# Optimization experiments

Hardware: AMD Instinct MI355X
Metric: run time of the kernel (lower is better)

Reference implementation:

```python
import jax, jax.numpy as jnp
import numpy as np

B, R, SR, K, F = 1, 2048, 24, 8, 32
DIST_FREQ = 2   # dist_xyz_freq -> PE dim 2*2*3 = 12
VIEW_FREQ = 4   # num_viewdir_freqs -> PE dim 2*4*3 = 24


def pe(x, n_freqs):
    # positional encoding: concat sin/cos of x * 2^i, flattened over last dim
    fb = (2.0 ** jnp.arange(n_freqs)).astype(x.dtype)          # [L]
    xb = x[..., None] * fb                                      # [..., 3, L]
    enc = jnp.concatenate([jnp.sin(xb), jnp.cos(xb)], axis=-1)  # [..., 3, 2L]
    return enc.reshape(*x.shape[:-1], -1)                       # [..., 3*2L]


def setup_inputs() -> dict:
    key = jax.random.key(0)
    ks = jax.random.split(key, 12)
    s = 0.1  # small init scale for weights
    return {
        'sampled_embedding': jax.random.normal(ks[0], (B, R, SR, K, F), jnp.float32),
        'dists': jax.random.normal(ks[1], (B, R, SR, K, 3), jnp.float32) * 0.1,
        'viewdirs': jax.random.normal(ks[2], (B, R, SR, 3), jnp.float32),
        'pnt_mask': jax.random.randint(ks[3], (B, R, SR, K), 0, 2, jnp.int32),
        'w1': jax.random.normal(ks[4], (F + 2 * DIST_FREQ * 3, 256), jnp.float32) * s,
        'b1': jnp.zeros((256,), jnp.float32),
        'w2': jax.random.normal(ks[5], (256, 256), jnp.float32) * s,
        'b2': jnp.zeros((256,), jnp.float32),
        'wa1': jax.random.normal(ks[6], (256, 256), jnp.float32) * s,
        'ba1': jnp.zeros((256,), jnp.float32),
        'wa2': jax.random.normal(ks[7], (256, 1), jnp.float32) * s,
        'ba2': jnp.zeros((1,), jnp.float32),
        'wc1': jax.random.normal(ks[8], (256 + 2 * VIEW_FREQ * 3, 256), jnp.float32) * s,
        'bc1': jnp.zeros((256,), jnp.float32),
        'wc2': jax.random.normal(ks[9], (256, 3), jnp.float32) * s,
        'bc2': jnp.zeros((3,), jnp.float32),
    }


def reference(sampled_embedding, dists, viewdirs, pnt_mask,
              w1, b1, w2, b2, wa1, ba1, wa2, ba2, wc1, bc1, wc2, bc2):
    mask = pnt_mask.astype(sampled_embedding.dtype)             # [B,R,SR,K]

    # quadric distance kernel -> normalized neighbor weights
    d2 = jnp.sum(dists * dists, axis=-1)                        # [B,R,SR,K]
    w = 1.0 / jnp.clip(d2, 1e-8)
    w = w * mask
    w = w / jnp.clip(jnp.sum(w, axis=-1, keepdims=True), 1e-8)  # agg_weight_norm

    # per-neighbor feature MLP (block1): feat ++ PE(dist_xyz) -> 256 -> 256
    feat_in = jnp.concatenate([sampled_embedding, pe(dists, DIST_FREQ)], axis=-1)
    h = jax.nn.relu(feat_in @ w1 + b1)
    h = jax.nn.relu(h @ w2 + b2)                                # [B,R,SR,K,256]

    # distance-weighted aggregation over neighbors (apply_pnt_mask folded into w)
    agg = jnp.einsum('brsk,brskc->brsc', w, h)                  # [B,R,SR,256]

    # alpha branch + raw2out_density (act_super: softplus(raw - 1))
    ah = jax.nn.relu(agg @ wa1 + ba1)
    density = jax.nn.softplus(ah @ wa2 + ba2 - 1.0)             # [B,R,SR,1]

    # color branch + raw2out_color (widened sigmoid)
    cin = jnp.concatenate([agg, pe(viewdirs, VIEW_FREQ)], axis=-1)
    ch = jax.nn.relu(cin @ wc1 + bc1)
    color = jax.nn.sigmoid(ch @ wc2 + bc2) * (1.0 + 2e-3) - 1e-3  # [B,R,SR,3]

    return jnp.concatenate([density, color], axis=-1)           # [B,R,SR,4]
```

## Files before the change

kernel.cpp:

```cpp
#include <hip/hip_runtime.h>

typedef unsigned short ushort_t;
typedef __bf16 bf16x8 __attribute__((ext_vector_type(8)));
typedef float f32x4 __attribute__((ext_vector_type(4)));

#define NPTS   49152
#define KNBR   8
#define PTS_A  8
#define NBLK_A (NPTS / PTS_A)
#define PTS_B  32
#define NBLK_B (NPTS / PTS_B)

#define W1S_OFF   0
#define W2S_OFF   16384
#define WA1S_OFF  81920
#define WC1S_OFF  147456
#define WA2S_OFF  221184
#define WC2S_OFF  225280
#define WS_WEIGHT 229376
#define AGG_OFF   229376

__device__ __forceinline__ float b2f(ushort_t u) {
    return __builtin_bit_cast(float, ((unsigned)u) << 16);
}
__device__ __forceinline__ ushort_t f2b(float f) {
    unsigned x = __builtin_bit_cast(unsigned, f);
    unsigned r = x + 0x7fffu + ((x >> 16) & 1u);
    return (ushort_t)(r >> 16);
}
__device__ __forceinline__ ushort_t f2bc(float f) {
    unsigned x = __builtin_bit_cast(unsigned, f);
    return (ushort_t)((x + 0x8000u) >> 16);
}

__global__ __launch_bounds__(256) void prep_swizzle(
    const float* __restrict__ w1, const float* __restrict__ w2,
    const float* __restrict__ wa1, const float* __restrict__ wc1,
    const float* __restrict__ wa2, const float* __restrict__ wc2,
    ushort_t* __restrict__ ws)
{
    int idx = blockIdx.x * 256 + threadIdx.x;
    if (idx >= WS_WEIGHT) return;

    if (idx >= WA2S_OFF) {
        int off2 = idx - WA2S_OFF;
        int mat = off2 >> 12;
        int off = off2 & 4095;
        int kb = off >> 7, rem = off & 127;
        int n = rem >> 3, j = rem & 7;
        int k = kb * 8 + j;
        float v = 0.f;
        if (mat == 0) { if (n == 0) v = wa2[k]; }
        else          { if (n < 3)  v = wc2[k * 3 + n]; }
        ws[idx] = f2b(v);
        return;
    }

    const float* src; int off, srcK, base;
    if (idx < W2S_OFF)        { src = w1;  base = W1S_OFF;  off = idx - W1S_OFF;  srcK = 44;  }
    else if (idx < WA1S_OFF)  { src = w2;  base = W2S_OFF;  off = idx - W2S_OFF;  srcK = 256; }
    else if (idx < WC1S_OFF)  { src = wa1; base = WA1S_OFF; off = idx - WA1S_OFF; srcK = 256; }
    else                      { src = wc1; base = WC1S_OFF; off = idx - WC1S_OFF; srcK = 280; }
    int kb  = off >> 11;
    int rem = off & 2047;
    int j = rem >> 8;
    int n = rem & 255;
    int k = kb * 8 + j;
    float v = (k < srcK) ? src[k * 256 + n] : 0.f;
    ws[base + kb * 2048 + n * 8 + j] = f2b(v);
}

__global__ __launch_bounds__(256) void pa_mlp(
    const float* __restrict__ emb, const float* __restrict__ dists,
    const int* __restrict__ mask,  const float* __restrict__ b1,
    const float* __restrict__ b2,  const ushort_t* __restrict__ ws,
    ushort_t* __restrict__ aggg)
{
    __shared__ __align__(16) ushort_t uH1[64 * 264];
    __shared__ __align__(16) float sWraw[64];
    __shared__ __align__(16) float sWn[64];
    ushort_t (*sFeat)[72] = (ushort_t(*)[72])uH1;
    ushort_t (*sH1)[264]  = (ushort_t(*)[264])uH1;

    const int tid  = threadIdx.x;
    const int lane = tid & 63;
    const int wv   = tid >> 6;
    const int n0   = lane & 15;
    const int quad = lane >> 4;
    const int pb   = blockIdx.x * PTS_A;
    const int colB = wv * 64;

    {
        int g0 = blockIdx.x * 2048 + tid * 8;
        int r = tid >> 2, c8 = (tid & 3) * 8;
        float4 f0 = *(const float4*)(emb + g0);
        float4 f1 = *(const float4*)(emb + g0 + 4);
        ushort_t v8[8];
        v8[0] = f2bc(f0.x); v8[1] = f2bc(f0.y); v8[2] = f2bc(f0.z); v8[3] = f2bc(f0.w);
        v8[4] = f2bc(f1.x); v8[5] = f2bc(f1.y); v8[6] = f2bc(f1.z); v8[7] = f2bc(f1.w);
        *(uint4*)&sFeat[r][c8] = *(uint4*)v8;
    }
    if (tid < 64) {
        int gr = pb * KNBR + tid;
        float x = dists[gr * 3 + 0];
        float y = dists[gr * 3 + 1];
        float z = dists[gr * 3 + 2];
        float d2 = x * x + y * y + z * z;
        sWraw[tid] = (float)mask[gr] / fmaxf(d2, 1e-8f);
        float xs[3] = {x, y, z};
        #pragma unroll
        for (int d = 0; d < 3; d++) {
            #pragma unroll
            for (int l = 0; l < 2; l++) {
                float ang = xs[d] * (float)(1 << l);
                sFeat[tid][32 + d * 4 + l]     = f2bc(__sinf(ang));
                sFeat[tid][32 + d * 4 + 2 + l] = f2bc(__cosf(ang));
            }
        }
        #pragma unroll
        for (int c = 44; c < 64; c++) sFeat[tid][c] = 0;
    }
    __syncthreads();
    if (tid < 64) {
        int lp = tid >> 3;
        float s = 0.f;
        #pragma unroll
        for (int k = 0; k < 8; k++) s += sWraw[lp * 8 + k];
        sWn[tid] = sWraw[tid] / fmaxf(s, 1e-8f);
    }

    f32x4 acc[16];
    #pragma unroll
    for (int i = 0; i < 16; i++) acc[i] = (f32x4){0.f, 0.f, 0.f, 0.f};

    #pragma unroll
    for (int ki = 0; ki < 2; ki++) {
        bf16x8 a[4];
        #pragma unroll
        for (int mt = 0; mt < 4; mt++)
            a[mt] = *(const bf16x8*)&sFeat[mt * 16 + n0][ki * 32 + quad * 8];
        const ushort_t* bp = ws + W1S_OFF + ki * 8192 + quad * 2048 + (colB + n0) * 8;
        #pragma unroll
        for (int nt = 0; nt < 4; nt++) {
            bf16x8 b = *(const bf16x8*)(bp + nt * 128);
            #pragma unroll
            for (int mt = 0; mt < 4; mt++)
                acc[mt * 4 + nt] = __builtin_amdgcn_mfma_f32_16x16x32_bf16(a[mt], b, acc[mt * 4 + nt], 0, 0, 0);
        }
    }
    __syncthreads();

    {
        #pragma unroll
        for (int nt = 0; nt < 4; nt++) {
            int col = colB + nt * 16 + n0;
            float bias = b1[col];
            #pragma unroll
            for (int mt = 0; mt < 4; mt++)
                #pragma unroll
                for (int r = 0; r < 4; r++)
                    sH1[mt * 16 + quad * 4 + r][col] = f2bc(fmaxf(acc[mt * 4 + nt][r] + bias, 0.f));
        }
    }
    __syncthreads();

    #pragma unroll
    for (int i = 0; i < 16; i++) acc[i] = (f32x4){0.f, 0.f, 0.f, 0.f};
    #pragma unroll
    for (int ki = 0; ki < 8; ki++) {
        bf16x8 a[4];
        #pragma unroll
        for (int mt = 0; mt < 4; mt++)
            a[mt] = *(const bf16x8*)&sH1[mt * 16 + n0][ki * 32 + quad * 8];
        const ushort_t* bp = ws + W2S_OFF + ki * 8192 + quad * 2048 + (colB + n0) * 8;
        #pragma unroll
        for (int nt = 0; nt < 4; nt++) {
            bf16x8 b = *(const bf16x8*)(bp + nt * 128);
            #pragma unroll
            for (int mt = 0; mt < 4; mt++)
                acc[mt * 4 + nt] = __builtin_amdgcn_mfma_f32_16x16x32_bf16(a[mt], b, acc[mt * 4 + nt], 0, 0, 0);
        }
    }
    {
        #pragma unroll
        for (int mt = 0; mt < 4; mt++) {
            f32x4 wn4 = *(const f32x4*)&sWn[mt * 16 + quad * 4];
            #pragma unroll
            for (int nt = 0; nt < 4; nt++) {
                int col = colB + nt * 16 + n0;
                float bias = b2[col];
                float s = fmaxf(acc[mt * 4 + nt][0] + bias, 0.f) * wn4[0]
                        + fmaxf(acc[mt * 4 + nt][1] + bias, 0.f) * wn4[1]
                        + fmaxf(acc[mt * 4 + nt][2] + bias, 0.f) * wn4[2]
                        + fmaxf(acc[mt * 4 + nt][3] + bias, 0.f) * wn4[3];
                s += __shfl_xor(s, 16);
                if ((quad & 1) == 0) {
                    int pt = pb + 2 * mt + (quad >> 1);
                    aggg[(size_t)pt * 256 + col] = f2bc(s);
                }
            }
        }
    }
}

__global__ __launch_bounds__(256) void pa_branch(
    const float* __restrict__ vdirs,
    const float* __restrict__ ba1v, const float* __restrict__ ba2v,
    const float* __restrict__ bc1v, const float* __restrict__ bc2v,
    const ushort_t* __restrict__ ws, const ushort_t* __restrict__ aggg,
    float* __restrict__ out)
{
    __shared__ __align__(16) ushort_t reg1[32 * 296];
    __shared__ __align__(16) ushort_t reg2[32 * 264];
    ushort_t (*sCin)[296] = (ushort_t(*)[296])reg1;
    ushort_t (*sAh)[264]  = (ushort_t(*)[264])reg1;
    ushort_t (*sCh)[264]  = (ushort_t(*)[264])reg2;

    const int tid  = threadIdx.x;
    const int lane = tid & 63;
    const int wv   = tid >> 6;
    const int n0   = lane & 15;
    const int quad = lane >> 4;
    const int pb   = blockIdx.x * PTS_B;
    const int colB = wv * 64;

    #pragma unroll
    for (int it = 0; it < 4; it++) {
        int idx = (tid + it * 256) * 8;
        uint4 v = *(const uint4*)(aggg + (size_t)pb * 256 + idx);
        *(uint4*)&sCin[idx >> 8][idx & 255] = v;
    }
    #pragma unroll
    for (int it = 0; it < 3; it++) {
        int t = tid + it * 256;
        int p = t / 24, j = t % 24;
        int d = j >> 3, jj = j & 7, l = jj & 3, isc = jj >> 2;
        float ang = vdirs[(pb + p) * 3 + d] * (float)(1 << l);
        sCin[p][256 + j] = f2bc(isc ? __cosf(ang) : __sinf(ang));
    }
    sCin[tid >> 3][280 + (tid & 7)] = 0;
    __syncthreads();

    f32x4 accA[8], accC[8];
    #pragma unroll
    for (int i = 0; i < 8; i++) { accA[i] = (f32x4){0.f, 0.f, 0.f, 0.f}; accC[i] = accA[i]; }

    #pragma unroll
    for (int ki = 0; ki < 8; ki++) {
        bf16x8 a0 = *(const bf16x8*)&sCin[n0][ki * 32 + quad * 8];
        bf16x8 a1 = *(const bf16x8*)&sCin[16 + n0][ki * 32 + quad * 8];
        const ushort_t* bp = ws + WA1S_OFF + ki * 8192 + quad * 2048 + (colB + n0) * 8;
        #pragma unroll
        for (int nt = 0; nt < 4; nt++) {
            bf16x8 b = *(const bf16x8*)(bp + nt * 128);
            accA[nt]     = __builtin_amdgcn_mfma_f32_16x16x32_bf16(a0, b, accA[nt], 0, 0, 0);
            accA[4 + nt] = __builtin_amdgcn_mfma_f32_16x16x32_bf16(a1, b, accA[4 + nt], 0, 0, 0);
        }
    }
    #pragma unroll
    for (int ki = 0; ki < 9; ki++) {
        bf16x8 a0 = *(const bf16x8*)&sCin[n0][ki * 32 + quad * 8];
        bf16x8 a1 = *(const bf16x8*)&sCin[16 + n0][ki * 32 + quad * 8];
        const ushort_t* bp = ws + WC1S_OFF + ki * 8192 + quad * 2048 + (colB + n0) * 8;
        #pragma unroll
        for (int nt = 0; nt < 4; nt++) {
            bf16x8 b = *(const bf16x8*)(bp + nt * 128);
            accC[nt]     = __builtin_amdgcn_mfma_f32_16x16x32_bf16(a0, b, accC[nt], 0, 0, 0);
            accC[4 + nt] = __builtin_amdgcn_mfma_f32_16x16x32_bf16(a1, b, accC[4 + nt], 0, 0, 0);
        }
    }
    __syncthreads();

    #pragma unroll
    for (int nt = 0; nt < 4; nt++) {
        int col = colB + nt * 16 + n0;
        float biasA = ba1v[col];
        float biasC = bc1v[col];
        #pragma unroll
        for (int mt = 0; mt < 2; mt++)
            #pragma unroll
            for (int r = 0; r < 4; r++) {
                int row = mt * 16 + quad * 4 + r;
                sAh[row][col] = f2bc(fmaxf(accA[mt * 4 + nt][r] + biasA, 0.f));
                sCh[row][col] = f2bc(fmaxf(accC[mt * 4 + nt][r] + biasC, 0.f));
            }
    }
    __syncthreads();

    {
        const int isColor = wv >> 1;
        const int baseM   = (wv & 1) * 16;
        const ushort_t* A = isColor ? &sCh[0][0] : &sAh[0][0];
        const ushort_t* B = ws + (isColor ? WC2S_OFF : WA2S_OFF);
        f32x4 acc4 = (f32x4){0.f, 0.f, 0.f, 0.f};
        #pragma unroll
        for (int ki = 0; ki < 8; ki++) {
            bf16x8 a = *(const bf16x8*)(A + (baseM + n0) * 264 + ki * 32 + quad * 8);
            bf16x8 b = *(const bf16x8*)(B + ki * 512 + quad * 128 + n0 * 8);
            acc4 = __builtin_amdgcn_mfma_f32_16x16x32_bf16(a, b, acc4, 0, 0, 0);
        }
        if (!isColor) {
            if (n0 == 0) {
                float ba2s = ba2v[0];
                #pragma unroll
                for (int r = 0; r < 4; r++) {
                    int gp = pb + baseM + quad * 4 + r;
                    float yv = acc4[r] + ba2s - 1.0f;
                    out[(size_t)gp * 4] = (yv > 20.f) ? yv : log1pf(expf(yv));
                }
            }
        } else {
            if (n0 < 3) {
                float bc2s = bc2v[n0];
                #pragma unroll
                for (int r = 0; r < 4; r++) {
                    int gp = pb + baseM + quad * 4 + r;
                    float sig = 1.f / (1.f + expf(-(acc4[r] + bc2s)));
                    out[(size_t)gp * 4 + 1 + n0] = sig * (1.0f + 2e-3f) - 1e-3f;
                }
            }
        }
    }
}

extern "C" void kernel_launch(void* const* d_in, const int* in_sizes, int n_in,
                              void* d_out, int out_size, void* d_ws, size_t ws_size,
                              hipStream_t stream) {
    const float* emb   = (const float*)d_in[0];
    const float* dists = (const float*)d_in[1];
    const float* vdir  = (const float*)d_in[2];
    const int*   mask  = (const int*)d_in[3];
    const float* w1    = (const float*)d_in[4];
    const float* b1    = (const float*)d_in[5];
    const float* w2    = (const float*)d_in[6];
    const float* b2    = (const float*)d_in[7];
    const float* wa1   = (const float*)d_in[8];
    const float* ba1   = (const float*)d_in[9];
    const float* wa2   = (const float*)d_in[10];
    const float* ba2   = (const float*)d_in[11];
    const float* wc1   = (const float*)d_in[12];
    const float* bc1   = (const float*)d_in[13];
    const float* wc2   = (const float*)d_in[14];
    const float* bc2   = (const float*)d_in[15];
    ushort_t* ws  = (ushort_t*)d_ws;
    float*    out = (float*)d_out;

    prep_swizzle<<<dim3((WS_WEIGHT + 255) / 256), dim3(256), 0, stream>>>(
        w1, w2, wa1, wc1, wa2, wc2, ws);
    pa_mlp<<<dim3(NBLK_A), dim3(256), 0, stream>>>(
        emb, dists, mask, b1, b2, ws, ws + AGG_OFF);
    pa_branch<<<dim3(NBLK_B), dim3(256), 0, stream>>>(
        vdir, ba1, ba2, bc1, bc2, ws, ws + AGG_OFF, out);
}
```

Before: 211.0 us.

## Make pa_mlp persistent with register-cached W2 and bias folded into W1

```diff
diff --git a/kernel.cpp b/kernel.cpp
--- a/kernel.cpp
+++ b/kernel.cpp
@@ -4,12 +4,13 @@
 typedef __bf16 bf16x8 __attribute__((ext_vector_type(8)));
 typedef float f32x4 __attribute__((ext_vector_type(4)));
 
-#define NPTS   49152
-#define KNBR   8
-#define PTS_A  8
-#define NBLK_A (NPTS / PTS_A)
-#define PTS_B  32
-#define NBLK_B (NPTS / PTS_B)
+#define NPTS    49152
+#define KNBR    8
+#define PTS_A   8
+#define PBLK_A  512
+#define ITERS_A 12
+#define PTS_B   32
+#define NBLK_B  (NPTS / PTS_B)
 
 #define W1S_OFF   0
 #define W2S_OFF   16384
@@ -34,7 +35,8 @@
 }
 
 __global__ __launch_bounds__(256) void prep_swizzle(
-    const float* __restrict__ w1, const float* __restrict__ w2,
+    const float* __restrict__ w1, const float* __restrict__ b1,
+    const float* __restrict__ w2,
     const float* __restrict__ wa1, const float* __restrict__ wc1,
     const float* __restrict__ wa2, const float* __restrict__ wc2,
     ushort_t* __restrict__ ws)
@@ -56,9 +58,20 @@
         return;
     }
 
-    const float* src; int off, srcK, base;
-    if (idx < W2S_OFF)        { src = w1;  base = W1S_OFF;  off = idx - W1S_OFF;  srcK = 44;  }
-    else if (idx < WA1S_OFF)  { src = w2;  base = W2S_OFF;  off = idx - W2S_OFF;  srcK = 256; }
+    int off, base;
+    if (idx < W2S_OFF) {
+        off = idx; base = W1S_OFF;
+        int kb = off >> 11, rem = off & 2047;
+        int j = rem >> 8, n = rem & 255;
+        int k = kb * 8 + j;
+        float v = 0.f;
+        if (k < 44)       v = w1[k * 256 + n];
+        else if (k == 44) v = b1[n];
+        ws[base + kb * 2048 + n * 8 + j] = f2b(v);
+        return;
+    }
+    const float* src; int srcK;
+    if (idx < WA1S_OFF)       { src = w2;  base = W2S_OFF;  off = idx - W2S_OFF;  srcK = 256; }
     else if (idx < WC1S_OFF)  { src = wa1; base = WA1S_OFF; off = idx - WA1S_OFF; srcK = 256; }
     else                      { src = wc1; base = WC1S_OFF; off = idx - WC1S_OFF; srcK = 280; }
     int kb  = off >> 11;
@@ -70,11 +83,10 @@
     ws[base + kb * 2048 + n * 8 + j] = f2b(v);
 }
 
-__global__ __launch_bounds__(256) void pa_mlp(
+__global__ __launch_bounds__(256, 2) void pa_mlp(
     const float* __restrict__ emb, const float* __restrict__ dists,
-    const int* __restrict__ mask,  const float* __restrict__ b1,
-    const float* __restrict__ b2,  const ushort_t* __restrict__ ws,
-    ushort_t* __restrict__ aggg)
+    const int* __restrict__ mask,  const float* __restrict__ b2,
+    const ushort_t* __restrict__ ws, ushort_t* __restrict__ aggg)
 {
     __shared__ __align__(16) ushort_t uH1[64 * 264];
     __shared__ __align__(16) float sWraw[64];
@@ -87,119 +99,129 @@
     const int wv   = tid >> 6;
     const int n0   = lane & 15;
     const int quad = lane >> 4;
-    const int pb   = blockIdx.x * PTS_A;
     const int colB = wv * 64;
 
-    {
-        int g0 = blockIdx.x * 2048 + tid * 8;
-        int r = tid >> 2, c8 = (tid & 3) * 8;
-        float4 f0 = *(const float4*)(emb + g0);
-        float4 f1 = *(const float4*)(emb + g0 + 4);
-        ushort_t v8[8];
-        v8[0] = f2bc(f0.x); v8[1] = f2bc(f0.y); v8[2] = f2bc(f0.z); v8[3] = f2bc(f0.w);
-        v8[4] = f2bc(f1.x); v8[5] = f2bc(f1.y); v8[6] = f2bc(f1.z); v8[7] = f2bc(f1.w);
-        *(uint4*)&sFeat[r][c8] = *(uint4*)v8;
-    }
-    if (tid < 64) {
-        int gr = pb * KNBR + tid;
-        float x = dists[gr * 3 + 0];
-        float y = dists[gr * 3 + 1];
-        float z = dists[gr * 3 + 2];
-        float d2 = x * x + y * y + z * z;
-        sWraw[tid] = (float)mask[gr] / fmaxf(d2, 1e-8f);
-        float xs[3] = {x, y, z};
-        #pragma unroll
-        for (int d = 0; d < 3; d++) {
-            #pragma unroll
-            for (int l = 0; l < 2; l++) {
-                float ang = xs[d] * (float)(1 << l);
-                sFeat[tid][32 + d * 4 + l]     = f2bc(__sinf(ang));
-                sFeat[tid][32 + d * 4 + 2 + l] = f2bc(__cosf(ang));
-            }
-        }
-        #pragma unroll
-        for (int c = 44; c < 64; c++) sFeat[tid][c] = 0;
-    }
-    __syncthreads();
-    if (tid < 64) {
-        int lp = tid >> 3;
-        float s = 0.f;
-        #pragma unroll
-        for (int k = 0; k < 8; k++) s += sWraw[lp * 8 + k];
-        sWn[tid] = sWraw[tid] / fmaxf(s, 1e-8f);
-    }
-
-    f32x4 acc[16];
-    #pragma unroll
-    for (int i = 0; i < 16; i++) acc[i] = (f32x4){0.f, 0.f, 0.f, 0.f};
-
-    #pragma unroll
-    for (int ki = 0; ki < 2; ki++) {
-        bf16x8 a[4];
-        #pragma unroll
-        for (int mt = 0; mt < 4; mt++)
-            a[mt] = *(const bf16x8*)&sFeat[mt * 16 + n0][ki * 32 + quad * 8];
-        const ushort_t* bp = ws + W1S_OFF + ki * 8192 + quad * 2048 + (colB + n0) * 8;
-        #pragma unroll
-        for (int nt = 0; nt < 4; nt++) {
-            bf16x8 b = *(const bf16x8*)(bp + nt * 128);
+    bf16x8 w2c[32];
+    #pragma unroll
+    for (int ki = 0; ki < 8; ki++)
+        #pragma unroll
+        for (int nt = 0; nt < 4; nt++)
+            w2c[ki * 4 + nt] = *(const bf16x8*)(ws + W2S_OFF + ki * 8192 + quad * 2048 + (colB + nt * 16 + n0) * 8);
+
+    #pragma unroll 1
+    for (int it = 0; it < ITERS_A; it++) {
+        const int blk = blockIdx.x * ITERS_A + it;
+        const int pb  = blk * PTS_A;
+
+        {
+            int g0 = blk * 2048 + tid * 8;
+            int r = tid >> 2, c8 = (tid & 3) * 8;
+            float4 f0 = *(const float4*)(emb + g0);
+            float4 f1 = *(const float4*)(emb + g0 + 4);
+            ushort_t v8[8];
+            v8[0] = f2bc(f0.x); v8[1] = f2bc(f0.y); v8[2] = f2bc(f0.z); v8[3] = f2bc(f0.w);
+            v8[4] = f2bc(f1.x); v8[5] = f2bc(f1.y); v8[6] = f2bc(f1.z); v8[7] = f2bc(f1.w);
+            *(uint4*)&sFeat[r][c8] = *(uint4*)v8;
+        }
+        if (tid < 64) {
+            int gr = pb * KNBR + tid;
+            float x = dists[gr * 3 + 0];
+            float y = dists[gr * 3 + 1];
+            float z = dists[gr * 3 + 2];
+            float d2 = x * x + y * y + z * z;
+            sWraw[tid] = (float)mask[gr] / fmaxf(d2, 1e-8f);
+            float xs[3] = {x, y, z};
+            #pragma unroll
+            for (int d = 0; d < 3; d++) {
+                #pragma unroll
+                for (int l = 0; l < 2; l++) {
+                    float ang = xs[d] * (float)(1 << l);
+                    sFeat[tid][32 + d * 4 + l]     = f2bc(__sinf(ang));
+                    sFeat[tid][32 + d * 4 + 2 + l] = f2bc(__cosf(ang));
+                }
+            }
+            sFeat[tid][44] = 0x3F80;
+            #pragma unroll
+            for (int c = 45; c < 64; c++) sFeat[tid][c] = 0;
+        }
+        __syncthreads();
+        if (tid < 64) {
+            int lp = tid >> 3;
+            float s = 0.f;
+            #pragma unroll
+            for (int k = 0; k < 8; k++) s += sWraw[lp * 8 + k];
+            sWn[tid] = sWraw[tid] / fmaxf(s, 1e-8f);
+        }
+
+        f32x4 acc[16];
+        #pragma unroll
+        for (int i = 0; i < 16; i++) acc[i] = (f32x4){0.f, 0.f, 0.f, 0.f};
+
+        #pragma unroll
+        for (int ki = 0; ki < 2; ki++) {
+            bf16x8 a[4];
             #pragma unroll
             for (int mt = 0; mt < 4; mt++)
-                acc[mt * 4 + nt] = __builtin_amdgcn_mfma_f32_16x16x32_bf16(a[mt], b, acc[mt * 4 + nt], 0, 0, 0);
-        }
-    }
-    __syncthreads();
-
-    {
-        #pragma unroll
-        for (int nt = 0; nt < 4; nt++) {
-            int col = colB + nt * 16 + n0;
-            float bias = b1[col];
-            #pragma unroll
-            for (int mt = 0; mt < 4; mt++)
-                #pragma unroll
-                for (int r = 0; r < 4; r++)
-                    sH1[mt * 16 + quad * 4 + r][col] = f2bc(fmaxf(acc[mt * 4 + nt][r] + bias, 0.f));
-        }
-    }
-    __syncthreads();
-
-    #pragma unroll
-    for (int i = 0; i < 16; i++) acc[i] = (f32x4){0.f, 0.f, 0.f, 0.f};
-    #pragma unroll
-    for (int ki = 0; ki < 8; ki++) {
-        bf16x8 a[4];
-        #pragma unroll
-        for (int mt = 0; mt < 4; mt++)
-            a[mt] = *(const bf16x8*)&sH1[mt * 16 + n0][ki * 32 + quad * 8];
-        const ushort_t* bp = ws + W2S_OFF + ki * 8192 + quad * 2048 + (colB + n0) * 8;
-        #pragma unroll
-        for (int nt = 0; nt < 4; nt++) {
-            bf16x8 b = *(const bf16x8*)(bp + nt * 128);
-            #pragma unroll
-            for (int mt = 0; mt < 4; mt++)
-                acc[mt * 4 + nt] = __builtin_amdgcn_mfma_f32_16x16x32_bf16(a[mt], b, acc[mt * 4 + nt], 0, 0, 0);
-        }
-    }
-    {
-        #pragma unroll
-        for (int mt = 0; mt < 4; mt++) {
-            f32x4 wn4 = *(const f32x4*)&sWn[mt * 16 + quad * 4];
+                a[mt] = *(const bf16x8*)&sFeat[mt * 16 + n0][ki * 32 + quad * 8];
+            const ushort_t* bp = ws + W1S_OFF + ki * 8192 + quad * 2048 + (colB + n0) * 8;
+            #pragma unroll
+            for (int nt = 0; nt < 4; nt++) {
+                bf16x8 b = *(const bf16x8*)(bp + nt * 128);
+                #pragma unroll
+                for (int mt = 0; mt < 4; mt++)
+                    acc[mt * 4 + nt] = __builtin_amdgcn_mfma_f32_16x16x32_bf16(a[mt], b, acc[mt * 4 + nt], 0, 0, 0);
+            }
+        }
+        __syncthreads();
+
+        {
             #pragma unroll
             for (int nt = 0; nt < 4; nt++) {
                 int col = colB + nt * 16 + n0;
-                float bias = b2[col];
-                float s = fmaxf(acc[mt * 4 + nt][0] + bias, 0.f) * wn4[0]
-                        + fmaxf(acc[mt * 4 + nt][1] + bias, 0.f) * wn4[1]
-                        + fmaxf(acc[mt * 4 + nt][2] + bias, 0.f) * wn4[2]
-                        + fmaxf(acc[mt * 4 + nt][3] + bias, 0.f) * wn4[3];
-                s += __shfl_xor(s, 16);
-                if ((quad & 1) == 0) {
-                    int pt = pb + 2 * mt + (quad >> 1);
-                    aggg[(size_t)pt * 256 + col] = f2bc(s);
+                #pragma unroll
+                for (int mt = 0; mt < 4; mt++)
+                    #pragma unroll
+                    for (int r = 0; r < 4; r++)
+                        sH1[mt * 16 + quad * 4 + r][col] = f2bc(fmaxf(acc[mt * 4 + nt][r], 0.f));
+            }
+        }
+        __syncthreads();
+
+        #pragma unroll
+        for (int i = 0; i < 16; i++) acc[i] = (f32x4){0.f, 0.f, 0.f, 0.f};
+        #pragma unroll
+        for (int ki = 0; ki < 8; ki++) {
+            bf16x8 a[4];
+            #pragma unroll
+            for (int mt = 0; mt < 4; mt++)
+                a[mt] = *(const bf16x8*)&sH1[mt * 16 + n0][ki * 32 + quad * 8];
+            #pragma unroll
+            for (int nt = 0; nt < 4; nt++)
+                #pragma unroll
+                for (int mt = 0; mt < 4; mt++)
+                    acc[mt * 4 + nt] = __builtin_amdgcn_mfma_f32_16x16x32_bf16(a[mt], w2c[ki * 4 + nt], acc[mt * 4 + nt], 0, 0, 0);
+        }
+        {
+            #pragma unroll
+            for (int mt = 0; mt < 4; mt++) {
+                f32x4 wn4 = *(const f32x4*)&sWn[mt * 16 + quad * 4];
+                #pragma unroll
+                for (int nt = 0; nt < 4; nt++) {
+                    int col = colB + nt * 16 + n0;
+                    float bias = b2[col];
+                    float s = fmaxf(acc[mt * 4 + nt][0] + bias, 0.f) * wn4[0]
+                            + fmaxf(acc[mt * 4 + nt][1] + bias, 0.f) * wn4[1]
+                            + fmaxf(acc[mt * 4 + nt][2] + bias, 0.f) * wn4[2]
+                            + fmaxf(acc[mt * 4 + nt][3] + bias, 0.f) * wn4[3];
+                    s += __shfl_xor(s, 16);
+                    if ((quad & 1) == 0) {
+                        int pt = pb + 2 * mt + (quad >> 1);
+                        aggg[(size_t)pt * 256 + col] = f2bc(s);
+                    }
                 }
             }
         }
+        __syncthreads();
     }
 }
 
@@ -346,9 +368,9 @@
     float*    out = (float*)d_out;
 
     prep_swizzle<<<dim3((WS_WEIGHT + 255) / 256), dim3(256), 0, stream>>>(
-        w1, w2, wa1, wc1, wa2, wc2, ws);
-    pa_mlp<<<dim3(NBLK_A), dim3(256), 0, stream>>>(
-        emb, dists, mask, b1, b2, ws, ws + AGG_OFF);
+        w1, b1, w2, wa1, wc1, wa2, wc2, ws);
+    pa_mlp<<<dim3(PBLK_A), dim3(256), 0, stream>>>(
+        emb, dists, mask, b2, ws, ws + AGG_OFF);
     pa_branch<<<dim3(NBLK_B), dim3(256), 0, stream>>>(
         vdir, ba1, ba2, bc1, bc2, ws, ws + AGG_OFF, out);
 }
```

New measurement: 224.8 us. 6.6% more time.
